# Performance work log

Hardware: AMD Instinct MI355X
Metric: run time of the kernel (lower is better)

## Reference

```python
import jax, jax.numpy as jnp
import numpy as np

# Keras GRUCell (reset_after=True, default in TF2) step
# Keras LSTMCell step (gate order i, f, c, o)
# Keras RNN masking semantics: at masked steps, states are frozen and the
# step output is the previous output (equivalent to freezing every layer's h).

def _gru_step(a, h, W, U, bi, br):
    gx = a @ W + bi          # [B, 3H] input projection
    gh = h @ U + br          # [B, 3H] recurrent projection (reset_after)
    xz, xr, xh = jnp.split(gx, 3, axis=-1)
    rz, rr, rh = jnp.split(gh, 3, axis=-1)
    z = jax.nn.sigmoid(xz + rz)
    r = jax.nn.sigmoid(xr + rr)
    hh = jnp.tanh(xh + r * rh)
    return z * h + (1.0 - z) * hh


def _lstm_step(a, h, c, W, U, b):
    g = a @ W + h @ U + b    # [B, 4H]
    gi, gf, gc, go = jnp.split(g, 4, axis=-1)
    i = jax.nn.sigmoid(gi)
    f = jax.nn.sigmoid(gf)
    cn = f * c + i * jnp.tanh(gc)
    hn = jax.nn.sigmoid(go) * jnp.tanh(cn)
    return hn, cn


def run_gru_stack(x, mask, layers):
    # x: [B,T,D], mask: [B,T] bool; layers: list of (W,U,bi,br)
    B = x.shape[0]
    H = layers[0][1].shape[0]
    xT = jnp.swapaxes(x, 0, 1)      # [T,B,D]
    mT = jnp.swapaxes(mask, 0, 1)   # [T,B]

    def step(hs, inp):
        xt, mt = inp
        a = xt
        new = []
        for (W, U, bi, br), h in zip(layers, hs):
            hn = _gru_step(a, h, W, U, bi, br)
            hn = jnp.where(mt[:, None], hn, h)  # freeze state under mask
            new.append(hn)
            a = hn
        return tuple(new), a

    h0 = tuple(jnp.zeros((B, H), x.dtype) for _ in layers)
    _, ys = jax.lax.scan(step, h0, (xT, mT))
    return jnp.swapaxes(ys, 0, 1)   # [B,T,H]


def run_lstm_stack(x, mask, layers):
    # layers: list of (W,U,b)
    B = x.shape[0]
    H = layers[0][1].shape[0]
    xT = jnp.swapaxes(x, 0, 1)
    mT = jnp.swapaxes(mask, 0, 1)

    def step(state, inp):
        xt, mt = inp
        a = xt
        new = []
        for (W, U, b), (h, c) in zip(layers, state):
            hn, cn = _lstm_step(a, h, c, W, U, b)
            hn = jnp.where(mt[:, None], hn, h)
            cn = jnp.where(mt[:, None], cn, c)
            new.append((hn, cn))
            a = hn
        return tuple(new), a

    s0 = tuple((jnp.zeros((B, H), x.dtype), jnp.zeros((B, H), x.dtype)) for _ in layers)
    _, ys = jax.lax.scan(step, s0, (xT, mT))
    return jnp.swapaxes(ys, 0, 1)


def _forward(x, lengths, g_W0, g_U0, g_bi0, g_br0, g_W1, g_U1, g_bi1, g_br1,
             l_W0, l_U0, l_b0, l_W1, l_U1, l_b1, out_W, out_b):
    T = x.shape[1]
    mask = jnp.arange(T)[None, :] < lengths[:, None]          # [B,T]
    o1 = run_gru_stack(x, mask, [(g_W0, g_U0, g_bi0, g_br0),
                                 (g_W1, g_U1, g_bi1, g_br1)])  # [B,T,H]
    o2 = run_lstm_stack(x, mask, [(l_W0, l_U0, l_b0),
                                  (l_W1, l_U1, l_b1)])          # [B,T,H]
    c = jnp.concatenate([o1, o2], axis=-1)                      # [B,T,2H]
    return c @ out_W + out_b                                    # [B,T,1]


def setup_inputs() -> dict:
    key = jax.random.key(0)
    ks = jax.random.split(key, 16)
    B, T, D, H = 64, 512, 96, 256
    glorot = lambda k, shp: (jax.random.normal(k, shp, dtype=jnp.float32)
                             / np.sqrt(shp[0]).astype(np.float32))
    inp = {
        "x": jax.random.normal(ks[0], (B, T, D), dtype=jnp.float32),
        "lengths": jax.random.randint(ks[1], (B,), 1, T + 1),
        # GRU stack (reset_after: separate input/recurrent biases)
        "g_W0": glorot(ks[2], (D, 3 * H)),
        "g_U0": glorot(ks[3], (H, 3 * H)),
        "g_bi0": jnp.zeros((3 * H,), jnp.float32),
        "g_br0": jnp.zeros((3 * H,), jnp.float32),
        "g_W1": glorot(ks[4], (H, 3 * H)),
        "g_U1": glorot(ks[5], (H, 3 * H)),
        "g_bi1": jnp.zeros((3 * H,), jnp.float32),
        "g_br1": jnp.zeros((3 * H,), jnp.float32),
        # LSTM stack
        "l_W0": glorot(ks[6], (D, 4 * H)),
        "l_U0": glorot(ks[7], (H, 4 * H)),
        "l_b0": jnp.zeros((4 * H,), jnp.float32),
        "l_W1": glorot(ks[8], (H, 4 * H)),
        "l_U1": glorot(ks[9], (H, 4 * H)),
        "l_b1": jnp.zeros((4 * H,), jnp.float32),
        # Dense head on concat [.., 2H] -> 1
        "out_W": glorot(ks[10], (2 * H, 1)),
        "out_b": jnp.zeros((1,), jnp.float32),
    }
    return inp


def reference(x, lengths, g_W0, g_U0, g_bi0, g_br0, g_W1, g_U1, g_bi1, g_br1,
              l_W0, l_U0, l_b0, l_W1, l_U1, l_b1, out_W, out_b):
    return _forward(x, lengths, g_W0, g_U0, g_bi0, g_br0, g_W1, g_U1, g_bi1,
                    g_br1, l_W0, l_U0, l_b0, l_W1, l_U1, l_b1, out_W, out_b)
```

## Files before the change

kernel.cpp:

```cpp
#include <hip/hip_runtime.h>
#include <hip/hip_fp16.h>

constexpr int Tt = 512, Dd = 96, Hh = 256;
constexpr int NS0 = 16;
constexpr int NSP = 8;
typedef unsigned long long u64;

constexpr size_t OFF_P0  = (size_t)4 << 20;
constexpr size_t OFF_P1  = (size_t)12 << 20;
constexpr size_t OFF_FLG = (size_t)20 << 20;
constexpr size_t OFF_W16 = ((size_t)20 << 20) + ((size_t)64 << 10);
constexpr size_t oGW0 = 0;
constexpr size_t oGU0 = oGW0 + (size_t)48 * 768;
constexpr size_t oGW1 = oGU0 + (size_t)128 * 768;
constexpr size_t oGU1 = oGW1 + (size_t)128 * 768;
constexpr size_t oLW0 = oGU1 + (size_t)128 * 768;
constexpr size_t oLU0 = oLW0 + (size_t)48 * 1024;
constexpr size_t oLW1 = oLU0 + (size_t)128 * 1024;
constexpr size_t oLU1 = oLW1 + (size_t)128 * 1024;

__device__ __forceinline__ float sigf(float v) { return 1.0f / (1.0f + __expf(-v)); }
__device__ __forceinline__ u64 agld(const u64* p) {
    return __hip_atomic_load(p, __ATOMIC_RELAXED, __HIP_MEMORY_SCOPE_AGENT);
}
__device__ __forceinline__ int agldi(const int* p) {
    return __hip_atomic_load(p, __ATOMIC_ACQUIRE, __HIP_MEMORY_SCOPE_AGENT);
}
__device__ __forceinline__ void agst(u64* p, u64 v) {
    __hip_atomic_store(p, v, __ATOMIC_RELAXED, __HIP_MEMORY_SCOPE_AGENT);
}

__device__ __forceinline__ float dot2f(unsigned w, unsigned a, float acc) {
#if __has_builtin(__builtin_amdgcn_fdot2)
    typedef _Float16 h2v __attribute__((ext_vector_type(2)));
    h2v wh, ah;
    __builtin_memcpy(&wh, &w, 4);
    __builtin_memcpy(&ah, &a, 4);
    return __builtin_amdgcn_fdot2(wh, ah, acc, false);
#else
    const float2 wf = __half22float2(*(const __half2*)&w);
    const float2 af = __half22float2(*(const __half2*)&a);
    acc = fmaf(wf.x, af.x, acc);
    return fmaf(wf.y, af.y, acc);
#endif
}

__device__ __forceinline__ int hidx(int k, int r) {
    return (k >> 1) * 8 + r * 2 + (k & 1);
}

template<int G>
__device__ __forceinline__ void load4h(uint4* wv, const uint4* __restrict__ M4,
                                       int ldm, int kpb) {
    const int base = (kpb >> 2) * ldm;
    #pragma unroll
    for (int g = 0; g < G; ++g)
        wv[g] = M4[base + g * 256];
}
template<int G>
__device__ __forceinline__ void fma4h(const uint4* wv, const uint4* __restrict__ A4,
                                      int kpb, float4* acc) {
    const uint4 a0 = A4[kpb + 0];
    const uint4 a1 = A4[kpb + 1];
    const uint4 a2 = A4[kpb + 2];
    const uint4 a3 = A4[kpb + 3];
    #pragma unroll
    for (int g = 0; g < G; ++g) {
        const uint4 w = wv[g];
        acc[g].x = dot2f(w.x, a0.x, acc[g].x);
        acc[g].y = dot2f(w.x, a0.y, acc[g].y);
        acc[g].z = dot2f(w.x, a0.z, acc[g].z);
        acc[g].w = dot2f(w.x, a0.w, acc[g].w);
        acc[g].x = dot2f(w.y, a1.x, acc[g].x);
        acc[g].y = dot2f(w.y, a1.y, acc[g].y);
        acc[g].z = dot2f(w.y, a1.z, acc[g].z);
        acc[g].w = dot2f(w.y, a1.w, acc[g].w);
        acc[g].x = dot2f(w.z, a2.x, acc[g].x);
        acc[g].y = dot2f(w.z, a2.y, acc[g].y);
        acc[g].z = dot2f(w.z, a2.z, acc[g].z);
        acc[g].w = dot2f(w.z, a2.w, acc[g].w);
        acc[g].x = dot2f(w.w, a3.x, acc[g].x);
        acc[g].y = dot2f(w.w, a3.y, acc[g].y);
        acc[g].z = dot2f(w.w, a3.z, acc[g].z);
        acc[g].w = dot2f(w.w, a3.w, acc[g].w);
    }
}
template<int G>
__device__ __forceinline__ void gemmP(const uint4* __restrict__ M4, int ldm,
                                      const uint4* __restrict__ A4,
                                      int kp0, int kp1, float4* acc) {
    const int n4 = (kp1 - kp0) >> 2;
    uint4 wv0[G], wv1[G];
    if (n4 <= 0) return;
    load4h<G>(wv0, M4, ldm, kp0);
    int c2 = 0;
    for (; c2 + 2 <= n4; c2 += 2) {
        load4h<G>(wv1, M4, ldm, kp0 + (c2 + 1) * 4);
        fma4h<G>(wv0, A4, kp0 + c2 * 4, acc);
        if (c2 + 2 < n4) load4h<G>(wv0, M4, ldm, kp0 + (c2 + 2) * 4);
        fma4h<G>(wv1, A4, kp0 + (c2 + 1) * 4, acc);
    }
    if (c2 < n4) fma4h<G>(wv0, A4, kp0 + c2 * 4, acc);
}

__global__ void cvt_pair(const float* __restrict__ src, unsigned* __restrict__ dst,
                         int n, int ld) {
    const int i = blockIdx.x * 256 + threadIdx.x;
    if (i >= n) return;
    const int kp = i / ld, col = i - kp * ld;
    const __half2 h = __floats2half2_rn(src[(2 * kp) * ld + col],
                                        src[(2 * kp + 1) * ld + col]);
    dst[((size_t)((kp >> 2) * ld + col) << 2) + (kp & 3)] = *(const unsigned*)&h;
}

__global__ void __launch_bounds__(1024, 4)
rnn_persist(const float* __restrict__ x, const int* __restrict__ lengths,
            const float* __restrict__ gbi0, const float* __restrict__ gbr0,
            const float* __restrict__ gbi1, const float* __restrict__ gbr1,
            const float* __restrict__ lb0, const float* __restrict__ lb1,
            const float* __restrict__ outW, const float* __restrict__ outb,
            float* __restrict__ out, char* __restrict__ wsb)
{
    const int tid = threadIdx.x;
    const int c   = tid & 255;
    const int grp = tid >> 8;
    const int bx  = blockIdx.x;
    const int role  = bx & 3;
    const int chain = (bx >> 2) & 1;
    const int rg    = bx >> 3;
    const int rowbase = rg * 4;

    const int GA  = chain ? 4 : 3;
    const int GAH = GA * Hh;

    u64* h0ring = (u64*)wsb + (size_t)(chain * 16 + rg) * (NS0 * 1024);
    u64* p0ring = (u64*)(wsb + OFF_P0) + (size_t)(chain * 16 + rg) * (NSP * 4096);
    u64* p1ring = (u64*)(wsb + OFF_P1) + (size_t)(chain * 16 + rg) * (NSP * 4096);
    int* flags = (int*)(wsb + OFF_FLG);
    int* flg_r0 = flags + ((chain * 16 + rg) * 4 + 1) * 32;
    int* flg_p1 = flags + ((chain * 16 + rg) * 4 + 2) * 32;
    int* flg_r1 = flags + ((chain * 16 + rg) * 4 + 3) * 32;

    const unsigned* W16 = (const unsigned*)(wsb + OFF_W16);
    size_t woff;
    if (chain == 0) woff = (role == 0) ? oGW0 : (role == 1) ? oGU0 : (role == 2) ? oGW1 : oGU1;
    else            woff = (role == 0) ? oLW0 : (role == 1) ? oLU0 : (role == 2) ? oLW1 : oLU1;
    const uint4* M4 = (const uint4*)(W16 + woff) + c;

    const int KR  = (role == 0) ? Dd : Hh;
    const int KP2 = KR >> 3;
    const int kp0 = grp * KP2, kp1 = kp0 + KP2;

    __shared__ __align__(16) unsigned sAh[128 * 4];
    __shared__ float sG[2 * 4096];
    __shared__ float sRed[16];
    __half* sAhh = (__half*)sAh;
    const uint4* A4 = (const uint4*)sAh;

    const int NP  = 4 * GAH;
    const int npt = NP >> 10;
    float biasv[4];
    int sgidx[4];
    if (role == 0 || role == 2) {
        const float* bsrc = (chain == 0) ? (role == 0 ? gbi0 : gbi1)
                                         : (role == 0 ? lb0 : lb1);
        #pragma unroll
        for (int i = 0; i < 4; ++i) {
            if (i < npt) {
                const int e = tid + i * 1024;
                const int r = e / GAH, rem = e - r * GAH;
                biasv[i] = bsrc[rem];
                sgidx[i] = r * 1024 + rem;
            } else { biasv[i] = 0; sgidx[i] = 0; }
        }
    }
    const int rA = grp;
    const int lenA = lengths[rowbase + rA];
    float brz = 0, brr = 0, brh = 0, ow = 0;
    if (chain == 0 && (role == 1 || role == 3)) {
        const float* br = (role == 1) ? gbr0 : gbr1;
        brz = br[c]; brr = br[Hh + c]; brh = br[2 * Hh + c];
    }
    if (role == 3) ow = outW[chain * Hh + c];
    const float outb0 = outb[0];
    float creg = 0.0f;
    float hprev = 0.0f;

    for (int i = tid; i < 512; i += 1024) sAh[i] = 0;
    __syncthreads();

    for (int t = 0; t < Tt; ++t) {
        if (role == 0) {
            if (t >= NSP) {
                if (tid == 0)
                    while (agldi(flg_r0) < t - NSP + 1) __builtin_amdgcn_s_sleep(1);
                __syncthreads();
            }
            if (tid < 4 * Dd) {
                const int r = tid / Dd, k = tid - r * Dd;
                const float v = x[((size_t)(rowbase + r) * Tt + t) * Dd + k];
                sAhh[hidx(k, r)] = __float2half(v);
            }
            __syncthreads();
        } else if (role == 2) {
            const u64* p0 = h0ring + (size_t)(t & (NS0 - 1)) * 1024 + rA * 256 + c;
            const unsigned want = (unsigned)(t + 1);
            u64 v0;
            do { v0 = agld(p0); } while ((unsigned)v0 != want);
            sAhh[hidx(c, rA)] = __float2half(__uint_as_float((unsigned)(v0 >> 32)));
            __syncthreads();
            if (tid == 0)
                __hip_atomic_exchange(flg_p1, t + 1, __ATOMIC_RELEASE,
                                      __HIP_MEMORY_SCOPE_AGENT);
        }

        if (chain == 0) {
            float4 acc[3] = {{0,0,0,0},{0,0,0,0},{0,0,0,0}};
            gemmP<3>(M4, GAH, A4, kp0, kp1, acc);
            if (grp < 2) {
                #pragma unroll
                for (int g = 0; g < 3; ++g) {
                    sG[grp * 4096 + 0 + g * 256 + c]    = acc[g].x;
                    sG[grp * 4096 + 1024 + g * 256 + c] = acc[g].y;
                    sG[grp * 4096 + 2048 + g * 256 + c] = acc[g].z;
                    sG[grp * 4096 + 3072 + g * 256 + c] = acc[g].w;
                }
            }
            __syncthreads();
            if (grp >= 2) {
                const int b = (grp - 2) * 4096;
                #pragma unroll
                for (int g = 0; g < 3; ++g) {
                    sG[b + 0 + g * 256 + c]    += acc[g].x;
                    sG[b + 1024 + g * 256 + c] += acc[g].y;
                    sG[b + 2048 + g * 256 + c] += acc[g].z;
                    sG[b + 3072 + g * 256 + c] += acc[g].w;
                }
            }
        } else {
            float4 acc[4] = {{0,0,0,0},{0,0,0,0},{0,0,0,0},{0,0,0,0}};
            gemmP<4>(M4, GAH, A4, kp0, kp1, acc);
            if (grp < 2) {
                #pragma unroll
                for (int g = 0; g < 4; ++g) {
                    sG[grp * 4096 + 0 + g * 256 + c]    = acc[g].x;
                    sG[grp * 4096 + 1024 + g * 256 + c] = acc[g].y;
                    sG[grp * 4096 + 2048 + g * 256 + c] = acc[g].z;
                    sG[grp * 4096 + 3072 + g * 256 + c] = acc[g].w;
                }
            }
            __syncthreads();
            if (grp >= 2) {
                const int b = (grp - 2) * 4096;
                #pragma unroll
                for (int g = 0; g < 4; ++g) {
                    sG[b + 0 + g * 256 + c]    += acc[g].x;
                    sG[b + 1024 + g * 256 + c] += acc[g].y;
                    sG[b + 2048 + g * 256 + c] += acc[g].z;
                    sG[b + 3072 + g * 256 + c] += acc[g].w;
                }
            }
        }
        __syncthreads();

        if (role == 0 || role == 2) {
            if (role == 2 && t >= NSP) {
                if (tid == 0)
                    while (agldi(flg_r1) < t - NSP + 1) __builtin_amdgcn_s_sleep(1);
                __syncthreads();
            }
            u64* ring = (role == 0) ? p0ring : p1ring;
            u64* slot = ring + (size_t)(t & (NSP - 1)) * 4096;
            for (int i = 0; i < npt; ++i) {
                const float v = sG[sgidx[i]] + sG[4096 + sgidx[i]] + biasv[i];
                agst(slot + tid + i * 1024,
                     ((u64)__float_as_uint(v) << 32) | (unsigned)(t + 1));
            }
        } else {
            const u64* slot = ((role == 1) ? p0ring : p1ring)
                              + (size_t)(t & (NSP - 1)) * 4096 + rA * GAH + c;
            const unsigned want = (unsigned)(t + 1);
            float P_[4] = {0, 0, 0, 0};
            unsigned dm = 0;
            const unsigned full = (1u << GA) - 1u;
            while (dm != full) {
                #pragma unroll
                for (int g = 0; g < 4; ++g) {
                    if (g < GA && !(dm & (1u << g))) {
                        const u64 v = agld(slot + g * 256);
                        if ((unsigned)v == want) {
                            P_[g] = __uint_as_float((unsigned)(v >> 32));
                            dm |= 1u << g;
                        }
                    }
                }
            }
            if (role == 1 && t >= NS0) {
                if (tid == 0)
                    while (agldi(flg_p1) < t - NS0 + 1) __builtin_amdgcn_s_sleep(1);
                __syncthreads();
            }
            const int r = rA;
            const float hold = hprev;
            float hn;
            if (chain == 0) {
                const float Qz = sG[r * 1024 + c]       + sG[4096 + r * 1024 + c];
                const float Qr = sG[r * 1024 + 256 + c] + sG[4096 + r * 1024 + 256 + c];
                const float Qh = sG[r * 1024 + 512 + c] + sG[4096 + r * 1024 + 512 + c];
                const float z  = sigf(P_[0] + Qz + brz);
                const float rr = sigf(P_[1] + Qr + brr);
                const float hh = tanhf(P_[2] + rr * (Qh + brh));
                hn = z * hold + (1.0f - z) * hh;
                if (t >= lenA) hn = hold;
            } else {
                const float gi = P_[0] + sG[r * 1024 + c]       + sG[4096 + r * 1024 + c];
                const float gf = P_[1] + sG[r * 1024 + 256 + c] + sG[4096 + r * 1024 + 256 + c];
                const float gc = P_[2] + sG[r * 1024 + 512 + c] + sG[4096 + r * 1024 + 512 + c];
                const float go = P_[3] + sG[r * 1024 + 768 + c] + sG[4096 + r * 1024 + 768 + c];
                float cn = sigf(gf) * creg + sigf(gi) * tanhf(gc);
                hn = sigf(go) * tanhf(cn);
                if (t >= lenA) { hn = hold; cn = creg; }
                creg = cn;
            }
            hprev = hn;
            sAhh[hidx(c, r)] = __float2half(hn);
            if (role == 1) {
                agst(h0ring + (size_t)(t & (NS0 - 1)) * 1024 + r * 256 + c,
                     ((u64)__float_as_uint(hn) << 32) | (unsigned)(t + 1));
            } else {
                float vh = hn * ow;
                for (int o = 32; o > 0; o >>= 1)
                    vh += __shfl_down(vh, o);
                if ((tid & 63) == 0) sRed[tid >> 6] = vh;
                __syncthreads();
                if (tid < 4) {
                    const float s = sRed[tid * 4] + sRed[tid * 4 + 1]
                                  + sRed[tid * 4 + 2] + sRed[tid * 4 + 3];
                    atomicAdd(&out[(size_t)(rowbase + tid) * Tt + t],
                              s + (chain ? outb0 : 0.0f));
                }
            }
        }
        __syncthreads();
        if (tid == 0 && (role == 1 || role == 3)) {
            __hip_atomic_exchange((role == 1) ? flg_r0 : flg_r1, t + 1,
                                  __ATOMIC_RELEASE, __HIP_MEMORY_SCOPE_AGENT);
        }
    }
}

extern "C" void kernel_launch(void* const* d_in, const int* in_sizes, int n_in,
                              void* d_out, int out_size, void* d_ws, size_t ws_size,
                              hipStream_t stream) {
    const float* x       = (const float*)d_in[0];
    const int*   lengths = (const int*)d_in[1];
    const float* gW0  = (const float*)d_in[2];
    const float* gU0  = (const float*)d_in[3];
    const float* gbi0 = (const float*)d_in[4];
    const float* gbr0 = (const float*)d_in[5];
    const float* gW1  = (const float*)d_in[6];
    const float* gU1  = (const float*)d_in[7];
    const float* gbi1 = (const float*)d_in[8];
    const float* gbr1 = (const float*)d_in[9];
    const float* lW0  = (const float*)d_in[10];
    const float* lU0  = (const float*)d_in[11];
    const float* lb0  = (const float*)d_in[12];
    const float* lW1  = (const float*)d_in[13];
    const float* lU1  = (const float*)d_in[14];
    const float* lb1  = (const float*)d_in[15];
    const float* outW = (const float*)d_in[16];
    const float* outb = (const float*)d_in[17];
    float* out = (float*)d_out;
    char* wsb  = (char*)d_ws;

    hipMemsetAsync(d_ws, 0, OFF_FLG + (16 << 10), stream);
    hipMemsetAsync(d_out, 0, (size_t)out_size * sizeof(float), stream);

    unsigned* W16 = (unsigned*)(wsb + OFF_W16);
    struct { const float* s; size_t o; int K; int ld; } cv[8] = {
        {gW0, oGW0, 96, 768}, {gU0, oGU0, 256, 768},
        {gW1, oGW1, 256, 768}, {gU1, oGU1, 256, 768},
        {lW0, oLW0, 96, 1024}, {lU0, oLU0, 256, 1024},
        {lW1, oLW1, 256, 1024}, {lU1, oLU1, 256, 1024},
    };
    for (int i = 0; i < 8; ++i) {
        const int n = (cv[i].K / 2) * cv[i].ld;
        cvt_pair<<<(n + 255) / 256, 256, 0, stream>>>(cv[i].s, W16 + cv[i].o, n, cv[i].ld);
    }

    rnn_persist<<<dim3(128), dim3(1024), 0, stream>>>(
        x, lengths, gbi0, gbr0, gbi1, gbr1, lb0, lb1, outW, outb, out, wsb);
}
```

Before: 4.890 ms.

## Precompute layer-0 input projection, keep recurrent weights resident in LDS

The layer-0 input projection for all timesteps moves out of the recurrence into a separate fully parallel GEMM kernel over packed fp16 inputs. The persistent kernel is restructured so that each block keeps a slice of its recurrent weights resident in LDS. Layer 1 fuses W and U into one stacked matmul over [h0; h1]. Blocks are split across hidden units for 16 batch rows, with global h rings and flag-based backpressure. This removes the per-step producer/consumer ring for input projections and the weight refetch from global/L2, but adds a large P0 buffer in global memory and cross-block h exchange for every unit slice.

```diff
diff --git a/kernel.cpp b/kernel.cpp
--- a/kernel.cpp
+++ b/kernel.cpp
@@ -2,14 +2,13 @@
 #include <hip/hip_fp16.h>
 
 constexpr int Tt = 512, Dd = 96, Hh = 256;
-constexpr int NS0 = 16;
-constexpr int NSP = 8;
+constexpr int NS = 16;
 typedef unsigned long long u64;
 
-constexpr size_t OFF_P0  = (size_t)4 << 20;
-constexpr size_t OFF_P1  = (size_t)12 << 20;
-constexpr size_t OFF_FLG = (size_t)20 << 20;
-constexpr size_t OFF_W16 = ((size_t)20 << 20) + ((size_t)64 << 10);
+constexpr size_t OFF_H0  = 0;
+constexpr size_t OFF_H1  = (size_t)4 << 20;
+constexpr size_t OFF_FLG = (size_t)8 << 20;
+constexpr size_t OFF_W16 = (size_t)9 << 20;
 constexpr size_t oGW0 = 0;
 constexpr size_t oGU0 = oGW0 + (size_t)48 * 768;
 constexpr size_t oGW1 = oGU0 + (size_t)128 * 768;
@@ -18,6 +17,13 @@
 constexpr size_t oLU0 = oLW0 + (size_t)48 * 1024;
 constexpr size_t oLW1 = oLU0 + (size_t)128 * 1024;
 constexpr size_t oLU1 = oLW1 + (size_t)128 * 1024;
+constexpr size_t OFF_XP = (size_t)16 << 20;
+constexpr size_t OFF_PG = (size_t)32 << 20;
+constexpr size_t SZ_PG  = (size_t)64 * 512 * 768 * 4;
+constexpr size_t OFF_PL = OFF_PG + SZ_PG;
+constexpr size_t SZ_PL  = (size_t)64 * 512 * 1024 * 4;
+constexpr size_t WS_NEED = OFF_PL + SZ_PL;
+constexpr int LDS_BYTES = 155648;
 
 __device__ __forceinline__ float sigf(float v) { return 1.0f / (1.0f + __expf(-v)); }
 __device__ __forceinline__ u64 agld(const u64* p) {
@@ -28,6 +34,14 @@
 }
 __device__ __forceinline__ void agst(u64* p, u64 v) {
     __hip_atomic_store(p, v, __ATOMIC_RELAXED, __HIP_MEMORY_SCOPE_AGENT);
+}
+__device__ __forceinline__ void xrel(int* p, int v) {
+    __hip_atomic_exchange(p, v, __ATOMIC_RELEASE, __HIP_MEMORY_SCOPE_AGENT);
+}
+__device__ __forceinline__ float pollF(const u64* p, unsigned want) {
+    u64 v = agld(p);
+    while ((unsigned)v != want) v = agld(p);
+    return __uint_as_float((unsigned)(v >> 32));
 }
 
 __device__ __forceinline__ float dot2f(unsigned w, unsigned a, float acc) {
@@ -45,8 +59,17 @@
 #endif
 }
 
-__device__ __forceinline__ int hidx(int k, int r) {
-    return (k >> 1) * 8 + r * 2 + (k & 1);
+__device__ __forceinline__ void fmaC(const uint4 w, const uint4* __restrict__ A4,
+                                     int kpb, float4& a) {
+    const uint4 a0 = A4[kpb + 0], a1 = A4[kpb + 1], a2 = A4[kpb + 2], a3 = A4[kpb + 3];
+    a.x = dot2f(w.x, a0.x, a.x); a.y = dot2f(w.x, a0.y, a.y);
+    a.z = dot2f(w.x, a0.z, a.z); a.w = dot2f(w.x, a0.w, a.w);
+    a.x = dot2f(w.y, a1.x, a.x); a.y = dot2f(w.y, a1.y, a.y);
+    a.z = dot2f(w.y, a1.z, a.z); a.w = dot2f(w.y, a1.w, a.w);
+    a.x = dot2f(w.z, a2.x, a.x); a.y = dot2f(w.z, a2.y, a.y);
+    a.z = dot2f(w.z, a2.z, a.z); a.w = dot2f(w.z, a2.w, a.w);
+    a.x = dot2f(w.w, a3.x, a.x); a.y = dot2f(w.w, a3.y, a.y);
+    a.z = dot2f(w.w, a3.z, a.z); a.w = dot2f(w.w, a3.w, a.w);
 }
 
 template<int G>
@@ -60,30 +83,9 @@
 template<int G>
 __device__ __forceinline__ void fma4h(const uint4* wv, const uint4* __restrict__ A4,
                                       int kpb, float4* acc) {
-    const uint4 a0 = A4[kpb + 0];
-    const uint4 a1 = A4[kpb + 1];
-    const uint4 a2 = A4[kpb + 2];
-    const uint4 a3 = A4[kpb + 3];
     #pragma unroll
-    for (int g = 0; g < G; ++g) {
-        const uint4 w = wv[g];
-        acc[g].x = dot2f(w.x, a0.x, acc[g].x);
-        acc[g].y = dot2f(w.x, a0.y, acc[g].y);
-        acc[g].z = dot2f(w.x, a0.z, acc[g].z);
-        acc[g].w = dot2f(w.x, a0.w, acc[g].w);
-        acc[g].x = dot2f(w.y, a1.x, acc[g].x);
-        acc[g].y = dot2f(w.y, a1.y, acc[g].y);
-        acc[g].z = dot2f(w.y, a1.z, acc[g].z);
-        acc[g].w = dot2f(w.y, a1.w, acc[g].w);
-        acc[g].x = dot2f(w.z, a2.x, acc[g].x);
-        acc[g].y = dot2f(w.z, a2.y, acc[g].y);
-        acc[g].z = dot2f(w.z, a2.z, acc[g].z);
-        acc[g].w = dot2f(w.z, a2.w, acc[g].w);
-        acc[g].x = dot2f(w.w, a3.x, acc[g].x);
-        acc[g].y = dot2f(w.w, a3.y, acc[g].y);
-        acc[g].z = dot2f(w.w, a3.z, acc[g].z);
-        acc[g].w = dot2f(w.w, a3.w, acc[g].w);
-    }
+    for (int g = 0; g < G; ++g)
+        fmaC(wv[g], A4, kpb, acc[g]);
 }
 template<int G>
 __device__ __forceinline__ void gemmP(const uint4* __restrict__ M4, int ldm,
@@ -113,107 +115,53 @@
     dst[((size_t)((kp >> 2) * ld + col) << 2) + (kp & 3)] = *(const unsigned*)&h;
 }
 
+__global__ void pack_x(const float* __restrict__ x, unsigned* __restrict__ XP) {
+    const int i = blockIdx.x * 256 + threadIdx.x;
+    if (i >= 64 * Tt * 48) return;
+    const int kp = i % 48;
+    const int bt = i / 48;
+    const __half2 h = __floats2half2_rn(x[(size_t)bt * Dd + 2 * kp],
+                                        x[(size_t)bt * Dd + 2 * kp + 1]);
+    XP[i] = *(const unsigned*)&h;
+}
+
 __global__ void __launch_bounds__(1024, 4)
-rnn_persist(const float* __restrict__ x, const int* __restrict__ lengths,
-            const float* __restrict__ gbi0, const float* __restrict__ gbr0,
-            const float* __restrict__ gbi1, const float* __restrict__ gbr1,
-            const float* __restrict__ lb0, const float* __restrict__ lb1,
-            const float* __restrict__ outW, const float* __restrict__ outb,
-            float* __restrict__ out, char* __restrict__ wsb)
+gemm_p0(const unsigned* __restrict__ XP, const float* __restrict__ gbi0,
+        const float* __restrict__ lb0, char* __restrict__ wsb)
 {
     const int tid = threadIdx.x;
     const int c   = tid & 255;
     const int grp = tid >> 8;
     const int bx  = blockIdx.x;
-    const int role  = bx & 3;
-    const int chain = (bx >> 2) & 1;
-    const int rg    = bx >> 3;
+    const int tt = bx & 31, rg = (bx >> 5) & 15, chain = bx >> 9;
     const int rowbase = rg * 4;
-
-    const int GA  = chain ? 4 : 3;
+    const int GA = chain ? 4 : 3;
     const int GAH = GA * Hh;
-
-    u64* h0ring = (u64*)wsb + (size_t)(chain * 16 + rg) * (NS0 * 1024);
-    u64* p0ring = (u64*)(wsb + OFF_P0) + (size_t)(chain * 16 + rg) * (NSP * 4096);
-    u64* p1ring = (u64*)(wsb + OFF_P1) + (size_t)(chain * 16 + rg) * (NSP * 4096);
-    int* flags = (int*)(wsb + OFF_FLG);
-    int* flg_r0 = flags + ((chain * 16 + rg) * 4 + 1) * 32;
-    int* flg_p1 = flags + ((chain * 16 + rg) * 4 + 2) * 32;
-    int* flg_r1 = flags + ((chain * 16 + rg) * 4 + 3) * 32;
-
     const unsigned* W16 = (const unsigned*)(wsb + OFF_W16);
-    size_t woff;
-    if (chain == 0) woff = (role == 0) ? oGW0 : (role == 1) ? oGU0 : (role == 2) ? oGW1 : oGU1;
-    else            woff = (role == 0) ? oLW0 : (role == 1) ? oLU0 : (role == 2) ? oLW1 : oLU1;
-    const uint4* M4 = (const uint4*)(W16 + woff) + c;
-
-    const int KR  = (role == 0) ? Dd : Hh;
-    const int KP2 = KR >> 3;
-    const int kp0 = grp * KP2, kp1 = kp0 + KP2;
-
-    __shared__ __align__(16) unsigned sAh[128 * 4];
+    const uint4* M4 = (const uint4*)(W16 + (chain ? oLW0 : oGW0)) + c;
+    float* P0 = (float*)(wsb + (chain ? OFF_PL : OFF_PG));
+    const float* bsrc = chain ? lb0 : gbi0;
+
+    __shared__ __align__(16) unsigned sAh[512];
     __shared__ float sG[2 * 4096];
-    __shared__ float sRed[16];
-    __half* sAhh = (__half*)sAh;
     const uint4* A4 = (const uint4*)sAh;
-
-    const int NP  = 4 * GAH;
-    const int npt = NP >> 10;
-    float biasv[4];
-    int sgidx[4];
-    if (role == 0 || role == 2) {
-        const float* bsrc = (chain == 0) ? (role == 0 ? gbi0 : gbi1)
-                                         : (role == 0 ? lb0 : lb1);
-        #pragma unroll
-        for (int i = 0; i < 4; ++i) {
-            if (i < npt) {
-                const int e = tid + i * 1024;
-                const int r = e / GAH, rem = e - r * GAH;
-                biasv[i] = bsrc[rem];
-                sgidx[i] = r * 1024 + rem;
-            } else { biasv[i] = 0; sgidx[i] = 0; }
-        }
-    }
-    const int rA = grp;
-    const int lenA = lengths[rowbase + rA];
-    float brz = 0, brr = 0, brh = 0, ow = 0;
-    if (chain == 0 && (role == 1 || role == 3)) {
-        const float* br = (role == 1) ? gbr0 : gbr1;
-        brz = br[c]; brr = br[Hh + c]; brh = br[2 * Hh + c];
-    }
-    if (role == 3) ow = outW[chain * Hh + c];
-    const float outb0 = outb[0];
-    float creg = 0.0f;
-    float hprev = 0.0f;
-
-    for (int i = tid; i < 512; i += 1024) sAh[i] = 0;
-    __syncthreads();
-
-    for (int t = 0; t < Tt; ++t) {
-        if (role == 0) {
-            if (t >= NSP) {
-                if (tid == 0)
-                    while (agldi(flg_r0) < t - NSP + 1) __builtin_amdgcn_s_sleep(1);
-                __syncthreads();
-            }
-            if (tid < 4 * Dd) {
-                const int r = tid / Dd, k = tid - r * Dd;
-                const float v = x[((size_t)(rowbase + r) * Tt + t) * Dd + k];
-                sAhh[hidx(k, r)] = __float2half(v);
-            }
-            __syncthreads();
-        } else if (role == 2) {
-            const u64* p0 = h0ring + (size_t)(t & (NS0 - 1)) * 1024 + rA * 256 + c;
-            const unsigned want = (unsigned)(t + 1);
-            u64 v0;
-            do { v0 = agld(p0); } while ((unsigned)v0 != want);
-            sAhh[hidx(c, rA)] = __float2half(__uint_as_float((unsigned)(v0 >> 32)));
-            __syncthreads();
-            if (tid == 0)
-                __hip_atomic_exchange(flg_p1, t + 1, __ATOMIC_RELEASE,
-                                      __HIP_MEMORY_SCOPE_AGENT);
-        }
-
+    const int kp0 = grp * 12, kp1 = kp0 + 12;
+    const int npt = GA;
+    float biasv[4]; int rs[4], remv[4];
+    #pragma unroll
+    for (int i = 0; i < 4; ++i) {
+        if (i < npt) {
+            const int e = tid + i * 1024;
+            const int r = e / GAH, rem = e - r * GAH;
+            biasv[i] = bsrc[rem]; rs[i] = r; remv[i] = rem;
+        } else { biasv[i] = 0; rs[i] = 0; remv[i] = 0; }
+    }
+    for (int t = tt * 16; t < tt * 16 + 16; ++t) {
+        if (tid < 192) {
+            const int row = tid / 48, kp = tid - row * 48;
+            sAh[kp * 4 + row] = XP[((size_t)(rowbase + row) * Tt + t) * 48 + kp];
+        }
+        __syncthreads();
         if (chain == 0) {
             float4 acc[3] = {{0,0,0,0},{0,0,0,0},{0,0,0,0}};
             gemmP<3>(M4, GAH, A4, kp0, kp1, acc);
@@ -262,90 +210,273 @@
             }
         }
         __syncthreads();
-
-        if (role == 0 || role == 2) {
-            if (role == 2 && t >= NSP) {
-                if (tid == 0)
-                    while (agldi(flg_r1) < t - NSP + 1) __builtin_amdgcn_s_sleep(1);
-                __syncthreads();
-            }
-            u64* ring = (role == 0) ? p0ring : p1ring;
-            u64* slot = ring + (size_t)(t & (NSP - 1)) * 4096;
-            for (int i = 0; i < npt; ++i) {
-                const float v = sG[sgidx[i]] + sG[4096 + sgidx[i]] + biasv[i];
-                agst(slot + tid + i * 1024,
-                     ((u64)__float_as_uint(v) << 32) | (unsigned)(t + 1));
-            }
+        for (int i = 0; i < npt; ++i) {
+            const int idx = rs[i] * 1024 + remv[i];
+            const float v = sG[idx] + sG[4096 + idx] + biasv[i];
+            P0[((size_t)(rowbase + rs[i]) * Tt + t) * GAH + remv[i]] = v;
+        }
+        __syncthreads();
+    }
+}
+
+__global__ void __launch_bounds__(1024, 1)
+rnn_fused(const int* __restrict__ lengths, const float* __restrict__ gbr0,
+          const float* __restrict__ gbi1, const float* __restrict__ gbr1,
+          const float* __restrict__ lb1, const float* __restrict__ outW,
+          const float* __restrict__ outb, float* __restrict__ out,
+          char* __restrict__ wsb)
+{
+    extern __shared__ __align__(16) char smem[];
+    const int tid = threadIdx.x;
+    const int bx = blockIdx.x;
+    int chain, rq, us, kind;
+    if (bx < 32) { kind = 0; chain = bx >> 4; rq = (bx >> 2) & 3; us = bx & 3; }
+    else { const int i = bx - 32; kind = 1; chain = i >> 5; rq = (i >> 3) & 3; us = i & 7; }
+    const int rowbase = rq * 16;
+    const int GA = chain ? 4 : 3;
+    const int GAH = GA * 256;
+
+    u64* h0 = (u64*)(wsb + OFF_H0) + (size_t)chain * (NS * 16384);
+    u64* h1 = (u64*)(wsb + OFF_H1) + (size_t)chain * (NS * 16384);
+    int* flg = (int*)(wsb + OFF_FLG) + (chain * 4 + rq) * 1024;
+
+    const unsigned* W16 = (const unsigned*)(wsb + OFF_W16);
+    const int ld = chain ? 1024 : 768;
+
+    const int NC  = kind ? 128 : GA * 64;
+    const int WU4 = kind ? 64 * 128 : 32 * NC;
+    const int AQS = kind ? 256 : 128;
+    uint4* W4 = (uint4*)smem;
+    uint4* A4 = (uint4*)(smem + (size_t)WU4 * 16);
+    float* sG = (float*)(smem + (size_t)WU4 * 16 + (size_t)AQS * 4 * 16);
+    __half* sAhh = (__half*)A4;
+
+    if (kind == 0) {
+        const uint4* S = (const uint4*)(W16 + (chain ? oLU0 : oGU0));
+        for (int idx = tid; idx < WU4; idx += 1024) {
+            const int kpc = idx / NC, j = idx - kpc * NC;
+            const int gcol = (j >> 6) * 256 + us * 64 + (j & 63);
+            W4[idx] = S[(size_t)kpc * ld + gcol];
+        }
+    } else {
+        const uint4* SW = (const uint4*)(W16 + (chain ? oLW1 : oGW1));
+        const uint4* SU = (const uint4*)(W16 + (chain ? oLU1 : oGU1));
+        for (int idx = tid; idx < WU4; idx += 1024) {
+            const int kpc = idx >> 7, j = idx & 127;
+            const int g4 = j >> 5, u = j & 31;
+            const bool top = kpc < 32;
+            int sg;
+            if (chain) sg = g4;
+            else if (top) sg = (g4 == 3) ? -1 : g4;
+            else sg = (g4 == 2) ? -1 : ((g4 == 3) ? 2 : g4);
+            uint4 v = {0u, 0u, 0u, 0u};
+            if (sg >= 0) {
+                const uint4* S = top ? SW : SU;
+                v = S[(size_t)(top ? kpc : kpc - 32) * ld + sg * 256 + us * 32 + u];
+            }
+            W4[idx] = v;
+        }
+    }
+
+    const int uu   = kind ? (tid & 31) : (tid & 63);
+    const int urow = kind ? (tid >> 5) : (tid >> 6);
+    const bool upd = kind ? (tid < 512) : true;
+    const int uuG  = kind ? (us * 32 + uu) : (us * 64 + uu);
+    int len = 0; float b0 = 0, b1 = 0, b2 = 0, b3 = 0, ow = 0;
+    if (upd) {
+        len = lengths[rowbase + urow];
+        if (kind == 0) {
+            if (chain == 0) { b0 = gbr0[uuG]; b1 = gbr0[256 + uuG]; b2 = gbr0[512 + uuG]; }
         } else {
-            const u64* slot = ((role == 1) ? p0ring : p1ring)
-                              + (size_t)(t & (NSP - 1)) * 4096 + rA * GAH + c;
-            const unsigned want = (unsigned)(t + 1);
-            float P_[4] = {0, 0, 0, 0};
-            unsigned dm = 0;
-            const unsigned full = (1u << GA) - 1u;
-            while (dm != full) {
-                #pragma unroll
-                for (int g = 0; g < 4; ++g) {
-                    if (g < GA && !(dm & (1u << g))) {
-                        const u64 v = agld(slot + g * 256);
-                        if ((unsigned)v == want) {
-                            P_[g] = __uint_as_float((unsigned)(v >> 32));
-                            dm |= 1u << g;
-                        }
+            if (chain == 0) {
+                b0 = gbi1[uuG] + gbr1[uuG];
+                b1 = gbi1[256 + uuG] + gbr1[256 + uuG];
+                b2 = gbi1[512 + uuG];
+                b3 = gbr1[512 + uuG];
+            } else {
+                b0 = lb1[uuG]; b1 = lb1[256 + uuG];
+                b2 = lb1[512 + uuG]; b3 = lb1[768 + uuG];
+            }
+            ow = outW[chain * 256 + uuG];
+        }
+    }
+    const float outb0 = outb[0];
+    const float* P0 = (const float*)(wsb + (chain ? OFF_PL : OFF_PG));
+    float hprev = 0.0f, creg = 0.0f;
+
+    const int gc = kind ? (tid & 127) : (tid & 255);
+    const int gq = kind ? (tid >> 7) : (tid >> 8);
+    const bool gact = kind ? true : (gc < NC);
+
+    for (int i = tid; i < AQS * 4 * 4; i += 1024) ((unsigned*)A4)[i] = 0;
+    __syncthreads();
+
+    for (int t = 0; t < Tt; ++t) {
+        float p0r[4] = {0, 0, 0, 0};
+        if (kind == 0) {
+            const size_t pb = ((size_t)(rowbase + urow) * Tt + t) * GAH + uuG;
+            #pragma unroll
+            for (int g = 0; g < 4; ++g)
+                if (g < GA) p0r[g] = P0[pb + g * 256];
+        }
+
+        if (kind == 0) {
+            if (t > 0) {
+                const u64* base = h0 + (size_t)((t - 1) & (NS - 1)) * 16384;
+                const unsigned want = (unsigned)t;
+                #pragma unroll
+                for (int i = 0; i < 4; ++i) {
+                    const int p = tid + i * 1024;
+                    const int prow = p >> 8, pun = p & 255;
+                    const float v = pollF(base + (rowbase + prow) * 256 + pun, want);
+                    sAhh[(((prow >> 2) * 128 + (pun >> 1)) << 3) + ((prow & 3) << 1) + (pun & 1)]
+                        = __float2half(v);
+                }
+            }
+            __syncthreads();
+            if (tid == 0 && t > 0) xrel(flg + (0 + us) * 32, t);
+        } else {
+            {
+                const u64* base = h0 + (size_t)(t & (NS - 1)) * 16384;
+                const unsigned want = (unsigned)(t + 1);
+                #pragma unroll
+                for (int i = 0; i < 4; ++i) {
+                    const int p = tid + i * 1024;
+                    const int prow = p >> 8, pun = p & 255;
+                    const float v = pollF(base + (rowbase + prow) * 256 + pun, want);
+                    sAhh[(((prow >> 2) * 256 + (pun >> 1)) << 3) + ((prow & 3) << 1) + (pun & 1)]
+                        = __float2half(v);
+                }
+            }
+            if (t > 0) {
+                const u64* base = h1 + (size_t)((t - 1) & (NS - 1)) * 16384;
+                const unsigned want = (unsigned)t;
+                #pragma unroll
+                for (int i = 0; i < 4; ++i) {
+                    const int p = tid + i * 1024;
+                    const int prow = p >> 8, pun = p & 255;
+                    const float v = pollF(base + (rowbase + prow) * 256 + pun, want);
+                    sAhh[(((prow >> 2) * 256 + 128 + (pun >> 1)) << 3) + ((prow & 3) << 1) + (pun & 1)]
+                        = __float2half(v);
+                }
+            }
+            __syncthreads();
+            if (tid == 0) {
+                xrel(flg + (8 + us) * 32, t + 1);
+                if (t > 0) xrel(flg + (16 + us) * 32, t);
+            }
+        }
+
+        float4 a0 = {0,0,0,0}, a1 = a0, a2 = a0, a3 = a0;
+        if (gact) {
+            const uint4* Wc = W4 + gc;
+            const int kpcB = gq * 8;
+            for (int kpc = kpcB; kpc < kpcB + 8; ++kpc) {
+                const uint4 w = Wc[(size_t)kpc * NC];
+                fmaC(w, A4 + 0 * AQS, kpc * 4, a0);
+                fmaC(w, A4 + 1 * AQS, kpc * 4, a1);
+                fmaC(w, A4 + 2 * AQS, kpc * 4, a2);
+                fmaC(w, A4 + 3 * AQS, kpc * 4, a3);
+            }
+        }
+        if (gact && gq == 0) {
+            sG[gc*16+ 0]=a0.x; sG[gc*16+ 1]=a0.y; sG[gc*16+ 2]=a0.z; sG[gc*16+ 3]=a0.w;
+            sG[gc*16+ 4]=a1.x; sG[gc*16+ 5]=a1.y; sG[gc*16+ 6]=a1.z; sG[gc*16+ 7]=a1.w;
+            sG[gc*16+ 8]=a2.x; sG[gc*16+ 9]=a2.y; sG[gc*16+10]=a2.z; sG[gc*16+11]=a2.w;
+            sG[gc*16+12]=a3.x; sG[gc*16+13]=a3.y; sG[gc*16+14]=a3.z; sG[gc*16+15]=a3.w;
+        }
+        __syncthreads();
+        if (gact && gq != 0) {
+            atomicAdd(&sG[gc*16+ 0],a0.x); atomicAdd(&sG[gc*16+ 1],a0.y);
+            atomicAdd(&sG[gc*16+ 2],a0.z); atomicAdd(&sG[gc*16+ 3],a0.w);
+            atomicAdd(&sG[gc*16+ 4],a1.x); atomicAdd(&sG[gc*16+ 5],a1.y);
+            atomicAdd(&sG[gc*16+ 6],a1.z); atomicAdd(&sG[gc*16+ 7],a1.w);
+            atomicAdd(&sG[gc*16+ 8],a2.x); atomicAdd(&sG[gc*16+ 9],a2.y);
+            atomicAdd(&sG[gc*16+10],a2.z); atomicAdd(&sG[gc*16+11],a2.w);
+            atomicAdd(&sG[gc*16+12],a3.x); atomicAdd(&sG[gc*16+13],a3.y);
+            atomicAdd(&sG[gc*16+14],a3.z); atomicAdd(&sG[gc*16+15],a3.w);
+        }
+        __syncthreads();
+
+        float hn = 0.0f;
+        if (upd) {
+            float Q[4] = {0, 0, 0, 0};
+            if (kind == 0) {
+                #pragma unroll
+                for (int g = 0; g < 4; ++g)
+                    if (g < GA) Q[g] = sG[((g << 6) + uu) * 16 + urow];
+            } else {
+                #pragma unroll
+                for (int g = 0; g < 4; ++g)
+                    Q[g] = sG[((g << 5) + uu) * 16 + urow];
+            }
+            const float hold = hprev;
+            if (kind == 0) {
+                if (chain == 0) {
+                    const float z  = sigf(p0r[0] + Q[0] + b0);
+                    const float r_ = sigf(p0r[1] + Q[1] + b1);
+                    const float hh = tanhf(p0r[2] + r_ * (Q[2] + b2));
+                    hn = z * hold + (1.0f - z) * hh;
+                    if (t >= len) hn = hold;
+                } else {
+                    float cn = sigf(p0r[1] + Q[1]) * creg
+                             + sigf(p0r[0] + Q[0]) * tanhf(p0r[2] + Q[2]);
+                    hn = sigf(p0r[3] + Q[3]) * tanhf(cn);
+                    if (t >= len) { hn = hold; cn = creg; }
+                    creg = cn;
+                }
+            } else {
+                if (chain == 0) {
+                    const float z  = sigf(Q[0] + b0);
+                    const float r_ = sigf(Q[1] + b1);
+                    const float hh = tanhf(Q[2] + b2 + r_ * (Q[3] + b3));
+                    hn = z * hold + (1.0f - z) * hh;
+                    if (t >= len) hn = hold;
+                } else {
+                    float cn = sigf(Q[1] + b1) * creg
+                             + sigf(Q[0] + b0) * tanhf(Q[2] + b2);
+                    hn = sigf(Q[3] + b3) * tanhf(cn);
+                    if (t >= len) { hn = hold; cn = creg; }
+                    creg = cn;
+                }
+                float vh = hn * ow;
+                #pragma unroll
+                for (int o = 16; o > 0; o >>= 1) vh += __shfl_down(vh, o, 32);
+                if ((tid & 31) == 0)
+                    atomicAdd(&out[(size_t)(rowbase + urow) * Tt + t],
+                              vh + ((chain == 1 && us == 0) ? outb0 : 0.0f));
+            }
+            hprev = hn;
+        }
+
+        if (t >= NS) {
+            if (tid == 0) {
+                const int need = t - NS + 1;
+                if (kind == 0) {
+                    for (;;) {
+                        int m = 0x7fffffff;
+                        for (int f = 0; f < 4; ++f)  m = min(m, agldi(flg + f * 32));
+                        for (int f = 8; f < 16; ++f) m = min(m, agldi(flg + f * 32));
+                        if (m >= need) break;
+                        __builtin_amdgcn_s_sleep(1);
                     }
-                }
-            }
-            if (role == 1 && t >= NS0) {
-                if (tid == 0)
-                    while (agldi(flg_p1) < t - NS0 + 1) __builtin_amdgcn_s_sleep(1);
-                __syncthreads();
-            }
-            const int r = rA;
-            const float hold = hprev;
-            float hn;
-            if (chain == 0) {
-                const float Qz = sG[r * 1024 + c]       + sG[4096 + r * 1024 + c];
-                const float Qr = sG[r * 1024 + 256 + c] + sG[4096 + r * 1024 + 256 + c];
-                const float Qh = sG[r * 1024 + 512 + c] + sG[4096 + r * 1024 + 512 + c];
-                const float z  = sigf(P_[0] + Qz + brz);
-                const float rr = sigf(P_[1] + Qr + brr);
-                const float hh = tanhf(P_[2] + rr * (Qh + brh));
-                hn = z * hold + (1.0f - z) * hh;
-                if (t >= lenA) hn = hold;
-            } else {
-                const float gi = P_[0] + sG[r * 1024 + c]       + sG[4096 + r * 1024 + c];
-                const float gf = P_[1] + sG[r * 1024 + 256 + c] + sG[4096 + r * 1024 + 256 + c];
-                const float gc = P_[2] + sG[r * 1024 + 512 + c] + sG[4096 + r * 1024 + 512 + c];
-                const float go = P_[3] + sG[r * 1024 + 768 + c] + sG[4096 + r * 1024 + 768 + c];
-                float cn = sigf(gf) * creg + sigf(gi) * tanhf(gc);
-                hn = sigf(go) * tanhf(cn);
-                if (t >= lenA) { hn = hold; cn = creg; }
-                creg = cn;
-            }
-            hprev = hn;
-            sAhh[hidx(c, r)] = __float2half(hn);
-            if (role == 1) {
-                agst(h0ring + (size_t)(t & (NS0 - 1)) * 1024 + r * 256 + c,
-                     ((u64)__float_as_uint(hn) << 32) | (unsigned)(t + 1));
-            } else {
-                float vh = hn * ow;
-                for (int o = 32; o > 0; o >>= 1)
-                    vh += __shfl_down(vh, o);
-                if ((tid & 63) == 0) sRed[tid >> 6] = vh;
-                __syncthreads();
-                if (tid < 4) {
-                    const float s = sRed[tid * 4] + sRed[tid * 4 + 1]
-                                  + sRed[tid * 4 + 2] + sRed[tid * 4 + 3];
-                    atomicAdd(&out[(size_t)(rowbase + tid) * Tt + t],
-                              s + (chain ? outb0 : 0.0f));
-                }
-            }
+                } else {
+                    for (;;) {
+                        int m = 0x7fffffff;
+                        for (int f = 16; f < 24; ++f) m = min(m, agldi(flg + f * 32));
+                        if (m >= need) break;
+                        __builtin_amdgcn_s_sleep(1);
+                    }
+                }
+            }
+            __syncthreads();
+        }
+        if (upd) {
+            u64* ring = kind ? h1 : h0;
+            agst(ring + (size_t)(t & (NS - 1)) * 16384 + (rowbase + urow) * 256 + uuG,
+                 ((u64)__float_as_uint(hn) << 32) | (unsigned)(t + 1));
         }
         __syncthreads();
-        if (tid == 0 && (role == 1 || role == 3)) {
-            __hip_atomic_exchange((role == 1) ? flg_r0 : flg_r1, t + 1,
-                                  __ATOMIC_RELEASE, __HIP_MEMORY_SCOPE_AGENT);
-        }
     }
 }
 
@@ -373,7 +504,7 @@
     float* out = (float*)d_out;
     char* wsb  = (char*)d_ws;
 
-    hipMemsetAsync(d_ws, 0, OFF_FLG + (16 << 10), stream);
+    hipMemsetAsync(d_ws, 0, OFF_W16, stream);
     hipMemsetAsync(d_out, 0, (size_t)out_size * sizeof(float), stream);
 
     unsigned* W16 = (unsigned*)(wsb + OFF_W16);
@@ -388,6 +519,13 @@
         cvt_pair<<<(n + 255) / 256, 256, 0, stream>>>(cv[i].s, W16 + cv[i].o, n, cv[i].ld);
     }
 
-    rnn_persist<<<dim3(128), dim3(1024), 0, stream>>>(
-        x, lengths, gbi0, gbr0, gbi1, gbr1, lb0, lb1, outW, outb, out, wsb);
-}
+    unsigned* XP = (unsigned*)(wsb + OFF_XP);
+    const int nxp = 64 * Tt * 48;
+    pack_x<<<(nxp + 255) / 256, 256, 0, stream>>>(x, XP);
+    gemm_p0<<<dim3(1024), dim3(1024), 0, stream>>>(XP, gbi0, lb0, wsb);
+
+    (void)hipFuncSetAttribute((const void*)rnn_fused,
+                              hipFuncAttributeMaxDynamicSharedMemorySize, LDS_BYTES);
+    rnn_fused<<<dim3(96), dim3(1024), LDS_BYTES, stream>>>(
+        lengths, gbr0, gbi1, gbr1, lb1, outW, outb, out, wsb);
+}
```

New measurement: 15.44 ms. 3.16x slower.
